# Performance work log

Hardware: AMD Instinct MI355X
Metric: run time of the kernel (lower is better)

## Reference

```python
import jax, jax.numpy as jnp
import numpy as np
from jax.scipy.ndimage import map_coordinates

ANGLES = 180
PROJ = 180
IMG = 256
THETA_RAD = np.deg2rad(np.linspace(0.0, 180.0, ANGLES, endpoint=False)).astype(np.float32)


def _ramp_filter(size):
    # skimage _get_fourier_filter(size, 'ramp')
    n = np.concatenate((np.arange(1, size // 2 + 1, 2),
                        np.arange(size // 2 - 1, 0, -2)))
    f = np.zeros(size)
    f[0] = 0.25
    f[1::2] = -1.0 / (np.pi * n) ** 2
    return (2.0 * np.real(np.fft.fft(f))).astype(np.float32)


def radon_t(img, theta):
    # skimage radon(circle=True): rotate by each angle (bilinear warp) and sum rows
    N = img.shape[0]
    center = N // 2
    y, x = jnp.mgrid[0:N, 0:N]
    x = x.astype(jnp.float32)
    y = y.astype(jnp.float32)

    def one(th):
        c, s = jnp.cos(th), jnp.sin(th)
        sx = c * x + s * y - center * (c + s - 1.0)   # source col
        sy = -s * x + c * y - center * (c - s - 1.0)  # source row
        rot = map_coordinates(img, [sy, sx], order=1, mode='constant', cval=0.0)
        return rot.sum(axis=0)  # sum over rows -> [N]

    cols = jax.vmap(one)(theta)  # [A, N]
    return cols.T                # [N, A] sinogram


def iradon_t(sino, theta):
    # skimage iradon(circle=True, filter='ramp', interpolation='linear')
    N, A = sino.shape
    pad = max(64, int(2 ** np.ceil(np.log2(2 * N))))
    filt = jnp.asarray(_ramp_filter(pad))
    proj = jnp.fft.fft(jnp.pad(sino, ((0, pad - N), (0, 0))), axis=0) * filt[:, None]
    filtered = jnp.real(jnp.fft.ifft(proj, axis=0)[:N, :]).astype(jnp.float32)  # [N, A]

    radius = N // 2
    xpr, ypr = jnp.mgrid[0:N, 0:N]
    xpr = (xpr - radius).astype(jnp.float32)
    ypr = (ypr - radius).astype(jnp.float32)

    def one(col, th):
        # detector coordinate t, shifted so index 0 corresponds to x[0] = -N//2
        t = ypr * jnp.cos(th) - xpr * jnp.sin(th) + radius
        i0 = jnp.floor(t).astype(jnp.int32)
        frac = t - i0
        v0 = col[jnp.clip(i0, 0, N - 1)]
        v1 = col[jnp.clip(i0 + 1, 0, N - 1)]
        val = (1.0 - frac) * v0 + frac * v1
        inb = (t >= 0.0) & (t <= N - 1.0)  # np.interp(..., left=0, right=0)
        return jnp.where(inb, val, 0.0)

    back = jax.vmap(one)(filtered.T, theta).sum(axis=0)  # [N, N]
    mask = (xpr ** 2 + ypr ** 2) <= radius ** 2
    return jnp.where(mask, back, 0.0) * (jnp.pi / (2.0 * A))


def setup_inputs() -> dict:
    key = jax.random.key(0)
    ks = jax.random.split(key, 7)
    scale = 1.0 / np.sqrt(PROJ)
    return {
        "x": jax.random.normal(ks[0], (4, 3, IMG, IMG), dtype=jnp.float32),
        "Wq": jax.random.normal(ks[1], (PROJ, PROJ), dtype=jnp.float32) * scale,
        "bq": jax.random.normal(ks[2], (PROJ,), dtype=jnp.float32) * scale,
        "Wk": jax.random.normal(ks[3], (PROJ, PROJ), dtype=jnp.float32) * scale,
        "bk": jax.random.normal(ks[4], (PROJ,), dtype=jnp.float32) * scale,
        "Wv": jax.random.normal(ks[5], (PROJ, PROJ), dtype=jnp.float32) * scale,
        "bv": jax.random.normal(ks[6], (PROJ,), dtype=jnp.float32) * scale,
    }


def reference(x, Wq, bq, Wk, bk, Wv, bv):
    B, C, H, W = x.shape
    theta = jnp.asarray(THETA_RAD)
    imgs = x.reshape(B * C, H, W)
    sino = jax.vmap(lambda im: radon_t(im, theta))(imgs)  # [BC, H, A]
    Q = sino @ Wq.T + bq
    K = sino @ Wk.T + bk
    V = sino @ Wv.T + bv
    scores = jax.nn.softmax(
        jnp.einsum('nij,nkj->nik', Q, K) / jnp.sqrt(jnp.float32(PROJ)), axis=-1)
    att = jnp.einsum('nik,nkj->nij', scores, V)            # [BC, H, A]
    rec = jax.vmap(lambda s: iradon_t(s, theta))(att)      # [BC, H, W]
    return rec.reshape(B, C, H, W)
```

## Files before the change

### kernel.cpp

```cpp
#include <hip/hip_runtime.h>

#define AANG 180
#define NN 256
#define BCH 12

#ifndef M_PI
#define M_PI 3.14159265358979323846
#endif

__device__ __forceinline__ int iclamp(int v, int lo, int hi) {
    return v < lo ? lo : (v > hi ? hi : v);
}

#define LSTR 259
#define LROWSMAX 130

__global__ __launch_bounds__(1024, 1)
void radon_kernel(const float* __restrict__ x, float* __restrict__ partial) {
    __shared__ float tile[LROWSMAX * LSTR];
    __shared__ float red[1024];
    int blk = blockIdx.x;
    int g = blk & 31;
    int h = (blk >> 5) & 1;
    int n = blk >> 6;
    int tid = threadIdx.x;
    int lx = tid & 255;
    int qid = tid >> 8;
    int R0 = h ? 127 : -1;
    int nrows = h ? 130 : 129;
    float Ylo = h ? 127.0f : -1.0f;
    float Yhi = h ? 255.0f : 126.0f;
    const float* img = x + (size_t)n * NN * NN;

    for (int rr = qid; rr < nrows; rr += 4) {
        int gr = R0 + rr;
        bool rok = (gr >= 0) && (gr < NN);
        const float* row = img + gr * NN;
        int gc = lx - 1;
        tile[rr * LSTR + lx] = (rok && gc >= 0) ? row[gc] : 0.0f;
        if (lx < 3) {
            int gc2 = 255 + lx;
            tile[rr * LSTR + 256 + lx] = (rok && gc2 < NN) ? row[gc2] : 0.0f;
        }
    }
    __syncthreads();

    float fx = (float)lx;
    int u0 = qid * 64;
    for (int aa = 0; aa < 6; ++aa) {
        int a = g + aa * 32;
        if (a >= AANG) break;
        float th = (float)((double)a * (M_PI / 180.0));
        float c = cosf(th), s = sinf(th);
        float kx = -128.0f * (c + s - 1.0f);
        float ky = -128.0f * (c - s - 1.0f);
        float xcon = c * fx + kx;
        float dcon = -s * fx + ky;
        float acc = 0.0f;
#pragma unroll 4
        for (int i = 0; i < 64; ++i) {
            float fy = (float)(u0 + i);
            float sy = __builtin_fmaf(c, fy, dcon);
            float sx = __builtin_fmaf(s, fy, xcon);
            float iyf = floorf(sy), ixf = floorf(sx);
            if (iyf >= Ylo && iyf <= Yhi && ixf >= -1.0f && ixf <= 255.0f) {
                float wy = sy - iyf, wx = sx - ixf;
                int lr = (int)iyf - R0;
                int lc = (int)ixf + 1;
                const float* t0 = &tile[lr * LSTR + lc];
                float v00 = t0[0], v01 = t0[1];
                float v10 = t0[LSTR], v11 = t0[LSTR + 1];
                float wx1 = 1.0f - wx, wy1 = 1.0f - wy;
                acc += wy1 * (wx1 * v00 + wx * v01) + wy * (wx1 * v10 + wx * v11);
            }
        }
        red[tid] = acc;
        __syncthreads();
        if (tid < 256) {
            float ssum = red[tid] + red[tid + 256] + red[tid + 512] + red[tid + 768];
            partial[(((size_t)h * BCH + n) * AANG + a) * NN + tid] = ssum;
        }
        __syncthreads();
    }
}

__global__ void wtrans_kernel(const float* __restrict__ Wq, const float* __restrict__ Wk,
                              const float* __restrict__ Wv, float* __restrict__ WqT,
                              float* __restrict__ WkT, float* __restrict__ WvT) {
    int idx = blockIdx.x * 256 + threadIdx.x;
    if (idx < AANG * AANG) {
        int p = idx / AANG;
        int j = idx - p * AANG;
        int src = j * AANG + p;
        WqT[idx] = Wq[src];
        WkT[idx] = Wk[src];
        WvT[idx] = Wv[src];
    }
}

__global__ void qkv_kernel(const float* __restrict__ partial,
                           const float* __restrict__ WqT, const float* __restrict__ bq,
                           const float* __restrict__ WkT, const float* __restrict__ bk,
                           const float* __restrict__ WvT, const float* __restrict__ bv,
                           float* __restrict__ Q, float* __restrict__ Kt,
                           float* __restrict__ V) {
    __shared__ float srow[4][AANG];
    int blk = blockIdx.x;
    int n = blk >> 6;
    int i0 = (blk & 63) * 4;
    int tid = threadIdx.x;
    const size_t HOFF = (size_t)BCH * AANG * NN;
    if (tid < AANG) {
        for (int r = 0; r < 4; ++r) {
            size_t idx = (((size_t)n) * AANG + tid) * NN + (i0 + r);
            srow[r][tid] = partial[idx] + partial[idx + HOFF];
        }
    }
    __syncthreads();
    if (tid < AANG) {
        int j = tid;
        float bqv = bq[j], bkv = bk[j], bvv = bv[j];
        float aq0 = bqv, aq1 = bqv, aq2 = bqv, aq3 = bqv;
        float ak0 = bkv, ak1 = bkv, ak2 = bkv, ak3 = bkv;
        float av0 = bvv, av1 = bvv, av2 = bvv, av3 = bvv;
        for (int p = 0; p < AANG; ++p) {
            float wq = WqT[p * AANG + j];
            float wk = WkT[p * AANG + j];
            float wv = WvT[p * AANG + j];
            float s0 = srow[0][p], s1 = srow[1][p], s2 = srow[2][p], s3 = srow[3][p];
            aq0 += s0 * wq; aq1 += s1 * wq; aq2 += s2 * wq; aq3 += s3 * wq;
            ak0 += s0 * wk; ak1 += s1 * wk; ak2 += s2 * wk; ak3 += s3 * wk;
            av0 += s0 * wv; av1 += s1 * wv; av2 += s2 * wv; av3 += s3 * wv;
        }
        size_t qb = ((size_t)(n * NN + i0)) * AANG + j;
        Q[qb] = aq0; Q[qb + AANG] = aq1; Q[qb + 2 * AANG] = aq2; Q[qb + 3 * AANG] = aq3;
        V[qb] = av0; V[qb + AANG] = av1; V[qb + 2 * AANG] = av2; V[qb + 3 * AANG] = av3;
        size_t kb = ((size_t)(n * AANG + j)) * NN + i0;
        Kt[kb] = ak0; Kt[kb + 1] = ak1; Kt[kb + 2] = ak2; Kt[kb + 3] = ak3;
    }
}

__global__ void attn_kernel(const float* __restrict__ Q, const float* __restrict__ Kt,
                            const float* __restrict__ V, float* __restrict__ att_t) {
    __shared__ float qrow0[AANG], qrow1[AANG];
    __shared__ float red0[NN], red1[NN];
    __shared__ float prob0[NN], prob1[NN];
    int blk = blockIdx.x;
    int n = blk >> 7;
    int i0 = (blk & 127) * 2;
    int tid = threadIdx.x;
    if (tid < AANG) {
        qrow0[tid] = Q[((size_t)(n * NN + i0)) * AANG + tid];
        qrow1[tid] = Q[((size_t)(n * NN + i0 + 1)) * AANG + tid];
    }
    __syncthreads();
    float dot0 = 0.0f, dot1 = 0.0f;
    for (int j = 0; j < AANG; ++j) {
        float kv = Kt[((size_t)(n * AANG + j)) * NN + tid];
        dot0 += qrow0[j] * kv;
        dot1 += qrow1[j] * kv;
    }
    float rs = sqrtf((float)AANG);
    float l0 = dot0 / rs, l1 = dot1 / rs;
    red0[tid] = l0; red1[tid] = l1;
    __syncthreads();
    for (int st = NN / 2; st > 0; st >>= 1) {
        if (tid < st) {
            red0[tid] = fmaxf(red0[tid], red0[tid + st]);
            red1[tid] = fmaxf(red1[tid], red1[tid + st]);
        }
        __syncthreads();
    }
    float mx0 = red0[0], mx1 = red1[0];
    __syncthreads();
    float e0 = expf(l0 - mx0), e1 = expf(l1 - mx1);
    red0[tid] = e0; red1[tid] = e1;
    __syncthreads();
    for (int st = NN / 2; st > 0; st >>= 1) {
        if (tid < st) {
            red0[tid] += red0[tid + st];
            red1[tid] += red1[tid + st];
        }
        __syncthreads();
    }
    float d0 = red0[0], d1 = red1[0];
    prob0[tid] = e0 / d0;
    prob1[tid] = e1 / d1;
    __syncthreads();
    if (tid < AANG) {
        float acc0 = 0.0f, acc1 = 0.0f;
        const float* vb = V + (size_t)n * NN * AANG + tid;
        for (int k = 0; k < NN; ++k) {
            float v = vb[(size_t)k * AANG];
            acc0 += prob0[k] * v;
            acc1 += prob1[k] * v;
        }
        size_t ob = ((size_t)(n * AANG + tid)) * NN + i0;
        att_t[ob] = acc0;
        att_t[ob + 1] = acc1;
    }
}

__global__ void filter_kernel(const float* __restrict__ att_t, float* __restrict__ filt) {
    __shared__ float col[NN];
    __shared__ float coef[128];
    int blk = blockIdx.x;
    int tid = threadIdx.x;
    col[tid] = att_t[(size_t)blk * NN + tid];
    if (tid < 128) {
        double d = (double)(2 * tid + 1);
        coef[tid] = (float)(-2.0 / (M_PI * M_PI * d * d));
    }
    __syncthreads();
    float acc = 0.5f * col[tid];
    for (int m = 0; m < 128; ++m) {
        int d = 2 * m + 1;
        float lo = (tid - d >= 0) ? col[tid - d] : 0.0f;
        float hi = (tid + d < NN) ? col[tid + d] : 0.0f;
        acc += coef[m] * (lo + hi);
    }
    filt[(size_t)blk * NN + tid] = acc;
}

#define ACH 12
__global__ void backproj_kernel(const float* __restrict__ filt, float* __restrict__ out) {
    __shared__ float cols[ACH][NN];
    __shared__ float cs[AANG], sn[AANG];
    int blk = blockIdx.x;
    int n = blk >> 8;
    int r = blk & 255;
    int tid = threadIdx.x;
    if (tid < AANG) {
        float th = (float)((double)tid * (M_PI / 180.0));
        cs[tid] = cosf(th);
        sn[tid] = sinf(th);
    }
    float xr = (float)(r - 128);
    float yr = (float)(tid - 128);
    float acc = 0.0f;
    const float* fb = filt + (size_t)n * AANG * NN;
    for (int ch = 0; ch < AANG / ACH; ++ch) {
        __syncthreads();
        for (int q = 0; q < ACH; ++q)
            cols[q][tid] = fb[(size_t)(ch * ACH + q) * NN + tid];
        __syncthreads();
        for (int q = 0; q < ACH; ++q) {
            int aa = ch * ACH + q;
            float t = yr * cs[aa] - xr * sn[aa] + 128.0f;
            float i0f = floorf(t);
            int i0 = (int)i0f;
            float frac = t - i0f;
            int c0 = iclamp(i0, 0, NN - 1);
            int c1 = iclamp(i0 + 1, 0, NN - 1);
            float val = (1.0f - frac) * cols[q][c0] + frac * cols[q][c1];
            if (t >= 0.0f && t <= 255.0f) acc += val;
        }
    }
    bool inside = (xr * xr + yr * yr) <= 16384.0f;
    out[(size_t)blk * NN + tid] = inside ? acc * (float)(M_PI / 360.0) : 0.0f;
}

extern "C" void kernel_launch(void* const* d_in, const int* in_sizes, int n_in,
                              void* d_out, int out_size, void* d_ws, size_t ws_size,
                              hipStream_t stream) {
    const float* x  = (const float*)d_in[0];
    const float* Wq = (const float*)d_in[1];
    const float* bq = (const float*)d_in[2];
    const float* Wk = (const float*)d_in[3];
    const float* bk = (const float*)d_in[4];
    const float* Wv = (const float*)d_in[5];
    const float* bv = (const float*)d_in[6];
    float* out = (float*)d_out;
    float* ws = (float*)d_ws;

    const size_t SZ = (size_t)BCH * NN * AANG;
    float* P     = ws;
    float* Q     = P + 2 * SZ;
    float* Kt    = Q + SZ;
    float* V     = Kt + SZ;
    float* att_t = V + SZ;
    float* WqT   = att_t;
    float* WkT   = WqT + AANG * AANG;
    float* WvT   = WkT + AANG * AANG;
    float* filt  = P;

    wtrans_kernel<<<(AANG * AANG + 255) / 256, 256, 0, stream>>>(Wq, Wk, Wv, WqT, WkT, WvT);
    radon_kernel<<<BCH * 2 * 32, 1024, 0, stream>>>(x, P);
    qkv_kernel<<<BCH * (NN / 4), 192, 0, stream>>>(P, WqT, bq, WkT, bk, WvT, bv, Q, Kt, V);
    attn_kernel<<<BCH * (NN / 2), NN, 0, stream>>>(Q, Kt, V, att_t);
    filter_kernel<<<BCH * AANG, NN, 0, stream>>>(att_t, filt);
    backproj_kernel<<<BCH * NN, NN, 0, stream>>>(filt, out);
}
```

Baseline: 477.2 us.

## Clip radon ray loops to valid range and tighten several kernels

In the radon kernel, each wave now computes the range of row indices whose sample coordinates can land inside the loaded tile, and loops only over that range. The reduction buffer is double-buffered so the trailing barrier per angle can be dropped. The QKV kernel processes 8 rows per block instead of 4 to reuse weight loads, and the attention softmax reductions switch from shared-memory tree loops to wave shuffles. The filter coefficients are computed in float instead of double. The aim is to skip out-of-bounds samples and cut barrier and reduction overhead, at the cost of extra setup math per angle and more registers in the QKV kernel.

```diff
diff --git a/kernel.cpp b/kernel.cpp
--- a/kernel.cpp
+++ b/kernel.cpp
@@ -18,7 +18,7 @@
 __global__ __launch_bounds__(1024, 1)
 void radon_kernel(const float* __restrict__ x, float* __restrict__ partial) {
     __shared__ float tile[LROWSMAX * LSTR];
-    __shared__ float red[1024];
+    __shared__ float red[2][1024];
     int blk = blockIdx.x;
     int g = blk & 31;
     int h = (blk >> 5) & 1;
@@ -30,6 +30,7 @@
     int nrows = h ? 130 : 129;
     float Ylo = h ? 127.0f : -1.0f;
     float Yhi = h ? 255.0f : 126.0f;
+    float Yhi1 = Yhi + 1.0f;
     const float* img = x + (size_t)n * NN * NN;
 
     for (int rr = qid; rr < nrows; rr += 4) {
@@ -46,7 +47,11 @@
     __syncthreads();
 
     float fx = (float)lx;
-    int u0 = qid * 64;
+    int wave = tid >> 6;
+    float fxA = (float)((wave & 3) * 64);
+    float fxB = fxA + 63.0f;
+    int uq0 = qid * 64, uq1 = uq0 + 64;
+
     for (int aa = 0; aa < 6; ++aa) {
         int a = g + aa * 32;
         if (a >= AANG) break;
@@ -56,10 +61,33 @@
         float ky = -128.0f * (c - s - 1.0f);
         float xcon = c * fx + kx;
         float dcon = -s * fx + ky;
+
+        float loY, hiY;
+        if (__builtin_fabsf(c) > 1e-5f) {
+            float dA = -s * fxA + ky, dB = -s * fxB + ky;
+            float t1 = (Ylo - dA) / c, t2 = (Yhi1 - dA) / c;
+            float t3 = (Ylo - dB) / c, t4 = (Yhi1 - dB) / c;
+            loY = fminf(fminf(t1, t2), fminf(t3, t4));
+            hiY = fmaxf(fmaxf(t1, t2), fmaxf(t3, t4));
+        } else { loY = 0.0f; hiY = 256.0f; }
+        float loX, hiX;
+        if (s > 1e-5f) {
+            float xA = c * fxA + kx, xB = c * fxB + kx;
+            float t1 = (-1.0f - xA) / s, t2 = (257.0f - xA) / s;
+            float t3 = (-1.0f - xB) / s, t4 = (257.0f - xB) / s;
+            loX = fminf(fminf(t1, t2), fminf(t3, t4));
+            hiX = fmaxf(fmaxf(t1, t2), fmaxf(t3, t4));
+        } else { loX = 0.0f; hiX = 256.0f; }
+        float loF = fmaxf(fmaxf(loY, loX) - 1.0f, 0.0f);
+        float hiF = fminf(fminf(hiY, hiX) + 2.0f, 256.0f);
+        int us = max(uq0, (int)loF);
+        int ue = min(uq1, (int)hiF);
+        us = __builtin_amdgcn_readfirstlane(us);
+        ue = __builtin_amdgcn_readfirstlane(ue);
+
         float acc = 0.0f;
-#pragma unroll 4
-        for (int i = 0; i < 64; ++i) {
-            float fy = (float)(u0 + i);
+        for (int u = us; u < ue; ++u) {
+            float fy = (float)u;
             float sy = __builtin_fmaf(c, fy, dcon);
             float sx = __builtin_fmaf(s, fy, xcon);
             float iyf = floorf(sy), ixf = floorf(sx);
@@ -74,13 +102,14 @@
                 acc += wy1 * (wx1 * v00 + wx * v01) + wy * (wx1 * v10 + wx * v11);
             }
         }
-        red[tid] = acc;
+        int pb = aa & 1;
+        red[pb][tid] = acc;
         __syncthreads();
         if (tid < 256) {
-            float ssum = red[tid] + red[tid + 256] + red[tid + 512] + red[tid + 768];
+            float ssum = red[pb][tid] + red[pb][tid + 256] + red[pb][tid + 512] +
+                         red[pb][tid + 768];
             partial[(((size_t)h * BCH + n) * AANG + a) * NN + tid] = ssum;
         }
-        __syncthreads();
     }
 }
 
@@ -104,14 +133,14 @@
                            const float* __restrict__ WvT, const float* __restrict__ bv,
                            float* __restrict__ Q, float* __restrict__ Kt,
                            float* __restrict__ V) {
-    __shared__ float srow[4][AANG];
-    int blk = blockIdx.x;
-    int n = blk >> 6;
-    int i0 = (blk & 63) * 4;
+    __shared__ float srow[8][AANG];
+    int blk = blockIdx.x;
+    int n = blk >> 5;
+    int i0 = (blk & 31) * 8;
     int tid = threadIdx.x;
     const size_t HOFF = (size_t)BCH * AANG * NN;
     if (tid < AANG) {
-        for (int r = 0; r < 4; ++r) {
+        for (int r = 0; r < 8; ++r) {
             size_t idx = (((size_t)n) * AANG + tid) * NN + (i0 + r);
             srow[r][tid] = partial[idx] + partial[idx + HOFF];
         }
@@ -119,36 +148,41 @@
     __syncthreads();
     if (tid < AANG) {
         int j = tid;
+        float aq[8], ak[8], av[8];
         float bqv = bq[j], bkv = bk[j], bvv = bv[j];
-        float aq0 = bqv, aq1 = bqv, aq2 = bqv, aq3 = bqv;
-        float ak0 = bkv, ak1 = bkv, ak2 = bkv, ak3 = bkv;
-        float av0 = bvv, av1 = bvv, av2 = bvv, av3 = bvv;
+        for (int r = 0; r < 8; ++r) { aq[r] = bqv; ak[r] = bkv; av[r] = bvv; }
         for (int p = 0; p < AANG; ++p) {
             float wq = WqT[p * AANG + j];
             float wk = WkT[p * AANG + j];
             float wv = WvT[p * AANG + j];
-            float s0 = srow[0][p], s1 = srow[1][p], s2 = srow[2][p], s3 = srow[3][p];
-            aq0 += s0 * wq; aq1 += s1 * wq; aq2 += s2 * wq; aq3 += s3 * wq;
-            ak0 += s0 * wk; ak1 += s1 * wk; ak2 += s2 * wk; ak3 += s3 * wk;
-            av0 += s0 * wv; av1 += s1 * wv; av2 += s2 * wv; av3 += s3 * wv;
-        }
-        size_t qb = ((size_t)(n * NN + i0)) * AANG + j;
-        Q[qb] = aq0; Q[qb + AANG] = aq1; Q[qb + 2 * AANG] = aq2; Q[qb + 3 * AANG] = aq3;
-        V[qb] = av0; V[qb + AANG] = av1; V[qb + 2 * AANG] = av2; V[qb + 3 * AANG] = av3;
+#pragma unroll
+            for (int r = 0; r < 8; ++r) {
+                float sv = srow[r][p];
+                aq[r] += sv * wq;
+                ak[r] += sv * wk;
+                av[r] += sv * wv;
+            }
+        }
+        for (int r = 0; r < 8; ++r) {
+            size_t qb = ((size_t)(n * NN + i0 + r)) * AANG + j;
+            Q[qb] = aq[r];
+            V[qb] = av[r];
+        }
         size_t kb = ((size_t)(n * AANG + j)) * NN + i0;
-        Kt[kb] = ak0; Kt[kb + 1] = ak1; Kt[kb + 2] = ak2; Kt[kb + 3] = ak3;
+        for (int r = 0; r < 8; ++r) Kt[kb + r] = ak[r];
     }
 }
 
 __global__ void attn_kernel(const float* __restrict__ Q, const float* __restrict__ Kt,
                             const float* __restrict__ V, float* __restrict__ att_t) {
     __shared__ float qrow0[AANG], qrow1[AANG];
-    __shared__ float red0[NN], red1[NN];
     __shared__ float prob0[NN], prob1[NN];
+    __shared__ float w0[4], w1[4];
     int blk = blockIdx.x;
     int n = blk >> 7;
     int i0 = (blk & 127) * 2;
     int tid = threadIdx.x;
+    int wid = tid >> 6;
     if (tid < AANG) {
         qrow0[tid] = Q[((size_t)(n * NN + i0)) * AANG + tid];
         qrow1[tid] = Q[((size_t)(n * NN + i0 + 1)) * AANG + tid];
@@ -160,30 +194,28 @@
         dot0 += qrow0[j] * kv;
         dot1 += qrow1[j] * kv;
     }
-    float rs = sqrtf((float)AANG);
-    float l0 = dot0 / rs, l1 = dot1 / rs;
-    red0[tid] = l0; red1[tid] = l1;
-    __syncthreads();
-    for (int st = NN / 2; st > 0; st >>= 1) {
-        if (tid < st) {
-            red0[tid] = fmaxf(red0[tid], red0[tid + st]);
-            red1[tid] = fmaxf(red1[tid], red1[tid + st]);
-        }
-        __syncthreads();
-    }
-    float mx0 = red0[0], mx1 = red1[0];
-    __syncthreads();
+    const float rs = 0.0745355992f;
+    float l0 = dot0 * rs, l1 = dot1 * rs;
+    float m0 = l0, m1 = l1;
+    for (int off = 32; off > 0; off >>= 1) {
+        m0 = fmaxf(m0, __shfl_xor(m0, off));
+        m1 = fmaxf(m1, __shfl_xor(m1, off));
+    }
+    if ((tid & 63) == 0) { w0[wid] = m0; w1[wid] = m1; }
+    __syncthreads();
+    float mx0 = fmaxf(fmaxf(w0[0], w0[1]), fmaxf(w0[2], w0[3]));
+    float mx1 = fmaxf(fmaxf(w1[0], w1[1]), fmaxf(w1[2], w1[3]));
     float e0 = expf(l0 - mx0), e1 = expf(l1 - mx1);
-    red0[tid] = e0; red1[tid] = e1;
-    __syncthreads();
-    for (int st = NN / 2; st > 0; st >>= 1) {
-        if (tid < st) {
-            red0[tid] += red0[tid + st];
-            red1[tid] += red1[tid + st];
-        }
-        __syncthreads();
-    }
-    float d0 = red0[0], d1 = red1[0];
+    float s0 = e0, s1 = e1;
+    for (int off = 32; off > 0; off >>= 1) {
+        s0 += __shfl_xor(s0, off);
+        s1 += __shfl_xor(s1, off);
+    }
+    __syncthreads();
+    if ((tid & 63) == 0) { w0[wid] = s0; w1[wid] = s1; }
+    __syncthreads();
+    float d0 = w0[0] + w0[1] + w0[2] + w0[3];
+    float d1 = w1[0] + w1[1] + w1[2] + w1[3];
     prob0[tid] = e0 / d0;
     prob1[tid] = e1 / d1;
     __syncthreads();
@@ -208,8 +240,8 @@
     int tid = threadIdx.x;
     col[tid] = att_t[(size_t)blk * NN + tid];
     if (tid < 128) {
-        double d = (double)(2 * tid + 1);
-        coef[tid] = (float)(-2.0 / (M_PI * M_PI * d * d));
+        float d = (float)(2 * tid + 1);
+        coef[tid] = -2.0f / ((float)(M_PI * M_PI) * d * d);
     }
     __syncthreads();
     float acc = 0.5f * col[tid];
@@ -286,7 +318,7 @@
 
     wtrans_kernel<<<(AANG * AANG + 255) / 256, 256, 0, stream>>>(Wq, Wk, Wv, WqT, WkT, WvT);
     radon_kernel<<<BCH * 2 * 32, 1024, 0, stream>>>(x, P);
-    qkv_kernel<<<BCH * (NN / 4), 192, 0, stream>>>(P, WqT, bq, WkT, bk, WvT, bv, Q, Kt, V);
+    qkv_kernel<<<BCH * (NN / 8), 256, 0, stream>>>(P, WqT, bq, WkT, bk, WvT, bv, Q, Kt, V);
     attn_kernel<<<BCH * (NN / 2), NN, 0, stream>>>(Q, Kt, V, att_t);
     filter_kernel<<<BCH * AANG, NN, 0, stream>>>(att_t, filt);
     backproj_kernel<<<BCH * NN, NN, 0, stream>>>(filt, out);
```

Measured after the change: 486.6 us. No clear change (+2.0%).
